# Kernel optimization log

Measured on AMD Instinct MI355X. Metric: run time of the kernel, lower is better.

## Reference

```python
import jax, jax.numpy as jnp
import numpy as np
from jax import lax

EMBED_DIM = 64
NUM_CODES = 512
NUM_HID = 128
NUM_RES_HID = 32
NUM_RES_LAYERS = 2
COMMIT_COST = 0.25
EPS = 1e-5


def conv1d(x, w, b=None, stride=1, pad=0):
    # x: [B,C,L], w: [O,I,K]
    y = lax.conv_general_dilated(x, w, (stride,), [(pad, pad)],
                                 dimension_numbers=('NCH', 'OIH', 'NCH'))
    if b is not None:
        y = y + b[None, :, None]
    return y


def conv_transpose1d(x, w, b, stride=2, pad=1):
    # torch ConvTranspose1d weight: [C_in, C_out, K]; express as fractionally-strided conv
    k = w.shape[-1]
    w2 = jnp.flip(w, axis=-1).transpose(1, 0, 2)  # [C_out, C_in, K]
    y = lax.conv_general_dilated(x, w2, (1,), [(k - 1 - pad, k - 1 - pad)],
                                 lhs_dilation=(stride,),
                                 dimension_numbers=('NCH', 'OIH', 'NCH'))
    return y + b[None, :, None]


def residual_stack(x, res_w1, res_w2):
    # res_w1: [L, R, H, 3], res_w2: [L, H, R, 1]
    for i in range(res_w1.shape[0]):
        h = conv1d(jax.nn.relu(x), res_w1[i], None, 1, 1)
        h = conv1d(jax.nn.relu(h), res_w2[i], None, 1, 0)
        x = x + h
    return jax.nn.relu(x)


def setup_inputs() -> dict:
    key = jax.random.key(0)
    ks = iter(jax.random.split(key, 32))
    B, T = 64, 8192
    H, R, D, K = NUM_HID, NUM_RES_HID, EMBED_DIM, NUM_CODES

    def w(k_, shape, fan_in):
        bound = 1.0 / np.sqrt(fan_in)
        return jax.random.uniform(k_, shape, jnp.float32, -bound, bound)

    inp = {
        'x': jax.random.normal(next(ks), (B, 1, T), jnp.float32),
        # encoder
        'enc_w1': w(next(ks), (H // 2, 1, 4), 1 * 4),
        'enc_b1': w(next(ks), (H // 2,), 1 * 4),
        'enc_w2': w(next(ks), (H, H // 2, 4), (H // 2) * 4),
        'enc_b2': w(next(ks), (H,), (H // 2) * 4),
        'enc_w3': w(next(ks), (H, H, 3), H * 3),
        'enc_b3': w(next(ks), (H,), H * 3),
        'enc_res_w1': w(next(ks), (NUM_RES_LAYERS, R, H, 3), H * 3),
        'enc_res_w2': w(next(ks), (NUM_RES_LAYERS, H, R, 1), R * 1),
        'enc_pre_w': w(next(ks), (D, H, 1), H),
        'enc_pre_b': w(next(ks), (D,), H),
        # codebook
        'codebook': jax.random.uniform(next(ks), (K, D), jnp.float32, -1.0 / K, 1.0 / K),
        # decoder
        'dec_w1': w(next(ks), (H, D, 3), D * 3),
        'dec_b1': w(next(ks), (H,), D * 3),
        'dec_res_w1': w(next(ks), (NUM_RES_LAYERS, R, H, 3), H * 3),
        'dec_res_w2': w(next(ks), (NUM_RES_LAYERS, H, R, 1), R * 1),
        'dec_t1_w': w(next(ks), (H, H // 2, 4), H * 4),   # ConvTranspose1d weight [Cin,Cout,K]
        'dec_t1_b': w(next(ks), (H // 2,), H * 4),
        'dec_t2_w': w(next(ks), (H // 2, 1, 4), (H // 2) * 4),
        'dec_t2_b': w(next(ks), (1,), (H // 2) * 4),
    }
    return inp


def vq_forward(z, codebook):
    # z: [B, D, L]
    B = z.shape[0]
    inputs = z.transpose(0, 2, 1)                       # [B, L, D]
    flat = inputs.reshape(-1, inputs.shape[-1])          # [N, D]
    # squared euclidean distances (argmin equals cdist p=2 argmin)
    d2 = (jnp.sum(flat * flat, axis=1, keepdims=True)
          - 2.0 * flat @ codebook.T
          + jnp.sum(codebook * codebook, axis=1))        # [N, K]
    idx = jnp.argmin(d2, axis=1)                         # [N]
    quant = codebook[idx].reshape(inputs.shape)          # gather == onehot @ codebook

    e_loss = jnp.mean((lax.stop_gradient(quant) - inputs) ** 2)
    q_loss = jnp.mean((quant - lax.stop_gradient(inputs)) ** 2)
    loss = q_loss + COMMIT_COST * e_loss

    quant_st = inputs + lax.stop_gradient(quant - inputs)  # straight-through

    n_tok = flat.shape[0]
    avg_probs = jnp.zeros((codebook.shape[0],), jnp.float32).at[idx].add(1.0) / n_tok
    perplexity = jnp.exp(-jnp.sum(avg_probs * jnp.log(avg_probs + 1e-10)))

    return quant_st.transpose(0, 2, 1), loss, idx.reshape(B, -1), perplexity


def reference(x, enc_w1, enc_b1, enc_w2, enc_b2, enc_w3, enc_b3,
              enc_res_w1, enc_res_w2, enc_pre_w, enc_pre_b, codebook,
              dec_w1, dec_b1, dec_res_w1, dec_res_w2,
              dec_t1_w, dec_t1_b, dec_t2_w, dec_t2_b):
    # RevIN normalize (stats detached)
    means = lax.stop_gradient(jnp.mean(x, axis=2, keepdims=True))
    stds = lax.stop_gradient(jnp.sqrt(jnp.var(x, axis=2, keepdims=True) + EPS))
    xn = (x - means) / stds

    # Encoder
    h = jax.nn.relu(conv1d(xn, enc_w1, enc_b1, 2, 1))
    h = jax.nn.relu(conv1d(h, enc_w2, enc_b2, 2, 1))
    h = conv1d(h, enc_w3, enc_b3, 1, 1)
    h = residual_stack(h, enc_res_w1, enc_res_w2)
    z = conv1d(h, enc_pre_w, enc_pre_b, 1, 0)            # [B, D, T/4]

    # VQ (eval mode: no noise, no EMA)
    quant, vq_loss, indices, perplexity = vq_forward(z, codebook)

    # Decoder
    d = conv1d(quant, dec_w1, dec_b1, 1, 1)
    d = residual_stack(d, dec_res_w1, dec_res_w2)
    d = jax.nn.relu(conv_transpose1d(d, dec_t1_w, dec_t1_b, 2, 1))
    x_recon = conv_transpose1d(d, dec_t2_w, dec_t2_b, 2, 1)

    # RevIN denormalize
    x_recon = x_recon * stds + means
    return x_recon, vq_loss, indices, perplexity
```

## Files before the change

### kernel.cpp

```cpp
#include <hip/hip_runtime.h>
#include <cmath>

#define NBATCH 64
#define NQB    16
#define TLEN   8192
#define LA     4096
#define LB     2048
#define HID    128
#define HHALF  64
#define RESCH  32
#define EMB    64
#define NCODE  512
#define NTOK   (NBATCH * LB)

#define DW_MEAN 0
#define DW_RSTD 64
#define DW_W1   128
#define DW_B1   384
#define DW_W2   448
#define DW_B2   33216
#define DW_W3   33344
#define DW_B3   82496
#define DW_RW1  82624
#define DW_RW2  107200
#define DW_PW   115392
#define DW_PB   123584

#define WS_FMEAN 327680
#define WS_FSTD  327744
#define WS_CNORM 327808
#define WS_CNT   328320
#define WS_SSE   328832

#define OFF_QUANT 2097152ull
#define OFF_D2Q   35651584ull
#define OFF_D3Q   69206016ull
#define OFF_S64Q  102760448ull
#define OFF_Z64Q  111149056ull
#define OFF_A32   69206016ull
#define OFF_S32   2097152ull
#define OFF_B32   2097152ull


__global__ __launch_bounds__(1024) void zero_kernel(float* p, int n) {
    int i = blockIdx.x * 1024 + threadIdx.x;
    if (i < n) p[i] = 0.f;
}

__global__ __launch_bounds__(256) void cvt_kernel(const float* __restrict__ src,
                                                  double* __restrict__ dst, int n) {
    int i = blockIdx.x * 256 + threadIdx.x;
    if (i < n) dst[i] = (double)src[i];
}

__global__ __launch_bounds__(256) void cnorm_kernel(const float* __restrict__ cb,
                                                    float* __restrict__ cnorm) {
    int k = blockIdx.x * 256 + threadIdx.x;
    if (k < NCODE) {
        float p0=0,p1=0,p2=0,p3=0,p4=0,p5=0,p6=0,p7=0;
        const float* cp = cb + k * EMB;
        #pragma unroll
        for (int d = 0; d < EMB; d += 8) {
            p0 = __fadd_rn(p0, __fmul_rn(cp[d],   cp[d]));
            p1 = __fadd_rn(p1, __fmul_rn(cp[d+1], cp[d+1]));
            p2 = __fadd_rn(p2, __fmul_rn(cp[d+2], cp[d+2]));
            p3 = __fadd_rn(p3, __fmul_rn(cp[d+3], cp[d+3]));
            p4 = __fadd_rn(p4, __fmul_rn(cp[d+4], cp[d+4]));
            p5 = __fadd_rn(p5, __fmul_rn(cp[d+5], cp[d+5]));
            p6 = __fadd_rn(p6, __fmul_rn(cp[d+6], cp[d+6]));
            p7 = __fadd_rn(p7, __fmul_rn(cp[d+7], cp[d+7]));
        }
        float s01 = __fadd_rn(p0, p1), s23 = __fadd_rn(p2, p3);
        float s45 = __fadd_rn(p4, p5), s67 = __fadd_rn(p6, p7);
        cnorm[k] = __fadd_rn(__fadd_rn(s01, s23), __fadd_rn(s45, s67));
    }
}

__global__ __launch_bounds__(256) void stats_kernel(const float* __restrict__ x,
                                                    double* dws, float* ws) {
    __shared__ float sx[TLEN];
    __shared__ double red[256];
    const int b = blockIdx.x, t = threadIdx.x;
    const float* xb = x + (size_t)b * TLEN;
    double s = 0.0;
    for (int i = t; i < TLEN; i += 256) { float v = xb[i]; sx[i] = v; s += (double)v; }
    red[t] = s; __syncthreads();
    for (int st = 128; st > 0; st >>= 1) { if (t < st) red[t] += red[t + st]; __syncthreads(); }
    double mean = red[0] / (double)TLEN;
    __syncthreads();
    double s2 = 0.0;
    for (int i = t; i < TLEN; i += 256) { double d = (double)sx[i] - mean; s2 = fma(d, d, s2); }
    red[t] = s2; __syncthreads();
    for (int st = 128; st > 0; st >>= 1) { if (t < st) red[t] += red[t + st]; __syncthreads(); }
    if (t == 0) {
        double stdv = sqrt(red[0] / (double)TLEN + 1e-5);
        dws[DW_MEAN + b] = mean;
        dws[DW_RSTD + b] = 1.0 / stdv;
        ws[WS_FMEAN + b] = (float)mean;
        ws[WS_FSTD + b]  = (float)stdv;
    }
}

__global__ __launch_bounds__(256) void fused12_kern(
        const float* __restrict__ x, const double* __restrict__ dws,
        double* __restrict__ out, int b0) {
    __shared__ double xt[262];
    __shared__ double s1e[64][65];
    __shared__ double s1o[64][65];
    __shared__ double lw1[256];
    __shared__ double lb1[64];
    const int bq = blockIdx.y;
    const int bg = b0 + bq;
    const int l0 = blockIdx.x * 64;
    const int tid = threadIdx.x;
    const double mean = dws[DW_MEAN + bg], rstd = dws[DW_RSTD + bg];
    const double* w2 = dws + DW_W2;
    const double* b2 = dws + DW_B2;

    if (tid < 256) lw1[tid] = dws[DW_W1 + tid];
    if (tid < 64)  lb1[tid] = dws[DW_B1 + tid];
    const int x_base = 4 * l0 - 3;
    const float* xb = x + (size_t)bg * TLEN;
    for (int i = tid; i < 262; i += 256) {
        int g = x_base + i;
        xt[i] = (g >= 0 && g < TLEN) ? ((double)xb[g] - mean) * rstd : 0.0;
    }
    __syncthreads();
    for (int i = tid; i < 64 * 130; i += 256) {
        int o = i / 130, pp = i - o * 130;
        int m = 2 * l0 - 1 + pp;
        double val = 0.0;
        if (m >= 0 && m < LA) {
            double a = lb1[o];
            #pragma unroll
            for (int k = 0; k < 4; k++) a = fma(lw1[o * 4 + k], xt[2 * pp + k], a);
            val = a > 0.0 ? a : 0.0;
        }
        if ((pp & 1) == 0) s1o[o][pp >> 1] = val;
        else               s1e[o][(pp - 1) >> 1] = val;
    }
    __syncthreads();
    const int lane = tid & 63;
    const int wave = tid >> 6;
    const int o0 = __builtin_amdgcn_readfirstlane(wave * 32);
    double acc[32];
    #pragma unroll
    for (int j = 0; j < 32; j++) acc[j] = b2[o0 + j];
    for (int c = 0; c < 64; c++) {
        double v0 = s1o[c][lane];
        double v1 = s1e[c][lane];
        double v2 = s1o[c][lane + 1];
        double v3 = s1e[c][lane + 1];
        #pragma unroll
        for (int j = 0; j < 32; j++) {
            const double* wp = w2 + ((size_t)(o0 + j) * 64 + c) * 4;
            double a = acc[j];
            a = fma(wp[0], v0, a);
            a = fma(wp[1], v1, a);
            a = fma(wp[2], v2, a);
            a = fma(wp[3], v3, a);
            acc[j] = a;
        }
    }
    #pragma unroll
    for (int j = 0; j < 32; j++) {
        double a = acc[j] > 0.0 ? acc[j] : 0.0;
        out[((size_t)bq * HID + o0 + j) * LB + l0 + lane] = a;
    }
}

template<int CIN, int COUT, int K, bool RELU_IN, bool ADD_RES, bool HAS_BIAS>
__global__ __launch_bounds__(256) void conv64_kern(
        const double* __restrict__ in, const double* __restrict__ w,
        const double* __restrict__ bias, const double* res, double* out) {
    constexpr int W = 64 + K - 1;
    __shared__ double st[CIN * W];
    const int b = blockIdx.y;
    const int l0 = blockIdx.x * 64;
    const int tid = threadIdx.x;
    const double* inb = in + (size_t)b * CIN * LB;
    for (int i = tid; i < CIN * W; i += 256) {
        int c = i / W, p = i - c * W;
        int g = l0 + p - (K / 2);
        double v = 0.0;
        if (g >= 0 && g < LB) {
            v = inb[(size_t)c * LB + g];
            if (RELU_IN) v = v > 0.0 ? v : 0.0;
        }
        st[i] = v;
    }
    __syncthreads();
    const int lane = tid & 63;
    const int wave = tid >> 6;
    constexpr int OPW = COUT / 4;
    const int o0 = __builtin_amdgcn_readfirstlane(wave * OPW);
    const int l = l0 + lane;
    double acc[OPW];
    #pragma unroll
    for (int j = 0; j < OPW; j++) acc[j] = HAS_BIAS ? bias[o0 + j] : 0.0;
    for (int c = 0; c < CIN; c++) {
        double v[K];
        #pragma unroll
        for (int k = 0; k < K; k++) v[k] = st[c * W + lane + k];
        #pragma unroll
        for (int j = 0; j < OPW; j++) {
            const double* wp = w + ((size_t)(o0 + j) * CIN + c) * K;
            #pragma unroll
            for (int k = 0; k < K; k++) acc[j] = fma(wp[k], v[k], acc[j]);
        }
    }
    #pragma unroll
    for (int j = 0; j < OPW; j++) {
        double a = acc[j];
        if (ADD_RES) a += res[((size_t)b * COUT + o0 + j) * LB + l];
        out[((size_t)b * COUT + o0 + j) * LB + l] = a;
    }
}

__global__ __launch_bounds__(256) void vq_kernel(
        const double* __restrict__ z64, const float* __restrict__ cbf,
        const float* __restrict__ cnorm,
        float* __restrict__ quant, float* __restrict__ idx_out,
        float* __restrict__ cnt, float* __restrict__ sse_acc, int b0) {
    __shared__ float s_m[4][64];
    __shared__ int   s_c[4][64];
    const int tid = threadIdx.x;
    const int tl = tid & 63;
    const int q = tid >> 6;
    const int nl = blockIdx.x * 64 + tl;
    const int bq = nl >> 11, l = nl & 2047;
    const int bg = b0 + bq;
    const double* zp = z64 + (size_t)bq * EMB * LB + l;
    float zv[EMB];
    #pragma unroll
    for (int d = 0; d < EMB; d++) zv[d] = (float)zp[(size_t)d * LB];

    float p0=0,p1=0,p2=0,p3=0,p4=0,p5=0,p6=0,p7=0;
    #pragma unroll
    for (int d = 0; d < EMB; d += 8) {
        p0 = __fadd_rn(p0, __fmul_rn(zv[d],   zv[d]));
        p1 = __fadd_rn(p1, __fmul_rn(zv[d+1], zv[d+1]));
        p2 = __fadd_rn(p2, __fmul_rn(zv[d+2], zv[d+2]));
        p3 = __fadd_rn(p3, __fmul_rn(zv[d+3], zv[d+3]));
        p4 = __fadd_rn(p4, __fmul_rn(zv[d+4], zv[d+4]));
        p5 = __fadd_rn(p5, __fmul_rn(zv[d+5], zv[d+5]));
        p6 = __fadd_rn(p6, __fmul_rn(zv[d+6], zv[d+6]));
        p7 = __fadd_rn(p7, __fmul_rn(zv[d+7], zv[d+7]));
    }
    const float A = __fadd_rn(__fadd_rn(__fadd_rn(p0,p1), __fadd_rn(p2,p3)),
                              __fadd_rn(__fadd_rn(p4,p5), __fadd_rn(p6,p7)));

    float m1 = 1e30f; int c1 = 0;
    const int c0 = __builtin_amdgcn_readfirstlane(q * 128);
    for (int ci = 0; ci < 128; ci++) {
        const int c = c0 + ci;
        const float* wp = cbf + c * EMB;
        float d0=0,d1=0,d2=0,d3=0,d4=0,d5=0,d6=0,d7=0;
        #pragma unroll
        for (int d = 0; d < EMB; d += 8) {
            d0 = fmaf(wp[d],   zv[d],   d0);
            d1 = fmaf(wp[d+1], zv[d+1], d1);
            d2 = fmaf(wp[d+2], zv[d+2], d2);
            d3 = fmaf(wp[d+3], zv[d+3], d3);
            d4 = fmaf(wp[d+4], zv[d+4], d4);
            d5 = fmaf(wp[d+5], zv[d+5], d5);
            d6 = fmaf(wp[d+6], zv[d+6], d6);
            d7 = fmaf(wp[d+7], zv[d+7], d7);
        }
        float dot = __fadd_rn(__fadd_rn(__fadd_rn(d0,d1), __fadd_rn(d2,d3)),
                              __fadd_rn(__fadd_rn(d4,d5), __fadd_rn(d6,d7)));
        float m = __fadd_rn(__fsub_rn(A, __fmul_rn(2.0f, dot)), cnorm[c]);
        if (m < m1) { m1 = m; c1 = c; }
    }
    s_m[q][tl] = m1; s_c[q][tl] = c1;
    __syncthreads();
    if (q == 0) {
        float bm = s_m[0][tl]; int bc = s_c[0][tl];
        #pragma unroll
        for (int qq = 1; qq < 4; qq++) {
            float mm = s_m[qq][tl];
            if (mm < bm) { bm = mm; bc = s_c[qq][tl]; }
        }
        idx_out[(size_t)bg * LB + l] = (float)bc;
        atomicAdd(&cnt[bc], 1.0f);
        float* qp = quant + (size_t)bg * EMB * LB + l;
        const float* cp = cbf + bc * EMB;
        float sse = 0.f;
        #pragma unroll
        for (int d = 0; d < EMB; d++) {
            float qv = cp[d];
            qp[(size_t)d * LB] = qv;
            float df = qv - zv[d];
            sse = fmaf(df, df, sse);
        }
        for (int off = 32; off > 0; off >>= 1) sse += __shfl_down(sse, off);
        if (tl == 0) atomicAdd(sse_acc, sse);
    }
}

template<int CIN, int COUT, int K, bool RELU_IN, bool RELU_OUT, bool ADD_RES, bool HAS_BIAS>
__global__ __launch_bounds__(256) void conv32_kern(
        const float* __restrict__ in, const float* __restrict__ w,
        const float* __restrict__ bias, const float* res, float* out) {
    constexpr int W = 64 + K - 1;
    __shared__ float st[CIN * W];
    const int b = blockIdx.y;
    const int l0 = blockIdx.x * 64;
    const int tid = threadIdx.x;
    const float* inb = in + (size_t)b * CIN * LB;
    for (int i = tid; i < CIN * W; i += 256) {
        int c = i / W, p = i - c * W;
        int g = l0 + p - (K / 2);
        float v = 0.f;
        if (g >= 0 && g < LB) {
            v = inb[(size_t)c * LB + g];
            if (RELU_IN) v = fmaxf(v, 0.f);
        }
        st[i] = v;
    }
    __syncthreads();
    const int lane = tid & 63;
    const int wave = tid >> 6;
    constexpr int OPW = COUT / 4;
    constexpr int NO = OPW < 16 ? OPW : 16;
    const int l = l0 + lane;
    for (int oc = 0; oc < OPW; oc += NO) {
        const int o0 = __builtin_amdgcn_readfirstlane(wave * OPW + oc);
        float acc[NO];
        #pragma unroll
        for (int j = 0; j < NO; j++) acc[j] = HAS_BIAS ? bias[o0 + j] : 0.f;
        for (int c = 0; c < CIN; c++) {
            float v[K];
            #pragma unroll
            for (int k = 0; k < K; k++) v[k] = st[c * W + lane + k];
            #pragma unroll
            for (int j = 0; j < NO; j++) {
                #pragma unroll
                for (int k = 0; k < K; k++)
                    acc[j] = fmaf(w[((o0 + j) * CIN + c) * K + k], v[k], acc[j]);
            }
        }
        #pragma unroll
        for (int j = 0; j < NO; j++) {
            float a = acc[j];
            if (ADD_RES) a += res[((size_t)b * COUT + o0 + j) * LB + l];
            if (RELU_OUT) a = fmaxf(a, 0.f);
            out[((size_t)b * COUT + o0 + j) * LB + l] = a;
        }
    }
}

__global__ __launch_bounds__(256) void convt1_kern(const float* __restrict__ in,
        const float* __restrict__ w, const float* __restrict__ bias, float* out) {
    __shared__ float s_in[HID * 66];
    const int b = blockIdx.y;
    const int t0 = blockIdx.x * 128;
    const int m0 = t0 / 2 - 1;
    const int tid = threadIdx.x;
    const float* inb = in + (size_t)b * HID * LB;
    for (int i = tid; i < HID * 66; i += 256) {
        int c = i / 66, p = i - c * 66;
        int m = m0 + p;
        s_in[i] = (m >= 0 && m < LB) ? fmaxf(inb[(size_t)c * LB + m], 0.f) : 0.f;
    }
    __syncthreads();
    const int lane = tid & 63;
    const int wave = tid >> 6;
    const int o0 = __builtin_amdgcn_readfirstlane(wave * 16);
    float accE[16], accO[16];
    #pragma unroll
    for (int j = 0; j < 16; j++) { float bv = bias[o0 + j]; accE[j] = bv; accO[j] = bv; }
    for (int c = 0; c < HID; c++) {
        float v0 = s_in[c * 66 + lane];
        float v1 = s_in[c * 66 + lane + 1];
        float v2 = s_in[c * 66 + lane + 2];
        #pragma unroll
        for (int j = 0; j < 16; j++) {
            const float* wc = w + ((size_t)c * HHALF + o0 + j) * 4;
            accE[j] = fmaf(wc[1], v1, fmaf(wc[3], v0, accE[j]));
            accO[j] = fmaf(wc[0], v2, fmaf(wc[2], v1, accO[j]));
        }
    }
    #pragma unroll
    for (int j = 0; j < 16; j++) {
        float2 pr;
        pr.x = fmaxf(accE[j], 0.f);
        pr.y = fmaxf(accO[j], 0.f);
        *(float2*)&out[((size_t)b * HHALF + o0 + j) * LA + t0 + 2 * lane] = pr;
    }
}

__global__ __launch_bounds__(256) void convt2_kern(const float* __restrict__ in,
        const float* __restrict__ w, const float* __restrict__ bias,
        const float* __restrict__ mstats, float* out) {
    __shared__ float s_in[16 * 258];
    const int b = blockIdx.y;
    const int t0 = blockIdx.x * 512;
    const int m0 = t0 / 2 - 1;
    const int tid = threadIdx.x;
    const float* inb = in + (size_t)b * HHALF * LA;
    float accE = 0.f, accO = 0.f;
    for (int cg = 0; cg < 4; cg++) {
        __syncthreads();
        for (int i = tid; i < 16 * 258; i += 256) {
            int c = i / 258, p = i - c * 258;
            int m = m0 + p;
            s_in[i] = (m >= 0 && m < LA) ? inb[(size_t)(cg * 16 + c) * LA + m] : 0.f;
        }
        __syncthreads();
        for (int c = 0; c < 16; c++) {
            float v0 = s_in[c * 258 + tid];
            float v1 = s_in[c * 258 + tid + 1];
            float v2 = s_in[c * 258 + tid + 2];
            const float* wc = w + (size_t)(cg * 16 + c) * 4;
            accE = fmaf(wc[1], v1, fmaf(wc[3], v0, accE));
            accO = fmaf(wc[0], v2, fmaf(wc[2], v1, accO));
        }
    }
    const float mean = mstats[WS_FMEAN + b], stdv = mstats[WS_FSTD + b];
    const float b0 = bias[0];
    float2 pr;
    pr.x = (accE + b0) * stdv + mean;
    pr.y = (accO + b0) * stdv + mean;
    *(float2*)&out[(size_t)b * TLEN + t0 + 2 * tid] = pr;
}

__global__ __launch_bounds__(512) void finalize_kernel(const float* cnt, const float* sse,
                                                       float* d_out) {
    __shared__ float red[512];
    const int t = threadIdx.x;
    float n = cnt[t];
    float p = n / (float)NTOK;
    red[t] = -p * logf(p + 1e-10f);
    __syncthreads();
    for (int s = 256; s > 0; s >>= 1) { if (t < s) red[t] += red[t + s]; __syncthreads(); }
    if (t == 0) {
        d_out[(size_t)NBATCH * TLEN] = sse[0] * 1.25f / (float)((size_t)NTOK * EMB);
        d_out[(size_t)NBATCH * TLEN + 1 + NTOK] = expf(red[0]);
    }
}

extern "C" void kernel_launch(void* const* d_in, const int* in_sizes, int n_in,
                              void* d_out, int out_size, void* d_ws, size_t ws_size,
                              hipStream_t stream) {
    (void)in_sizes; (void)n_in; (void)out_size; (void)ws_size;

    const float* x         = (const float*)d_in[0];
    const float* enc_w1    = (const float*)d_in[1];
    const float* enc_b1    = (const float*)d_in[2];
    const float* enc_w2    = (const float*)d_in[3];
    const float* enc_b2    = (const float*)d_in[4];
    const float* enc_w3    = (const float*)d_in[5];
    const float* enc_b3    = (const float*)d_in[6];
    const float* enc_rw1   = (const float*)d_in[7];
    const float* enc_rw2   = (const float*)d_in[8];
    const float* enc_pre_w = (const float*)d_in[9];
    const float* enc_pre_b = (const float*)d_in[10];
    const float* codebook  = (const float*)d_in[11];
    const float* dec_w1    = (const float*)d_in[12];
    const float* dec_b1    = (const float*)d_in[13];
    const float* dec_rw1   = (const float*)d_in[14];
    const float* dec_rw2   = (const float*)d_in[15];
    const float* dec_t1_w  = (const float*)d_in[16];
    const float* dec_t1_b  = (const float*)d_in[17];
    const float* dec_t2_w  = (const float*)d_in[18];
    const float* dec_t2_b  = (const float*)d_in[19];

    float*  ws  = (float*)d_ws;
    double* dws = (double*)d_ws;
    char*   wsb = (char*)d_ws;
    float*  out = (float*)d_out;

    float*  QUANT = (float*)(wsb + OFF_QUANT);
    double* D2Q   = (double*)(wsb + OFF_D2Q);
    double* D3Q   = (double*)(wsb + OFF_D3Q);
    double* S64Q  = (double*)(wsb + OFF_S64Q);
    double* Z64Q  = (double*)(wsb + OFF_Z64Q);
    float*  A32   = (float*)(wsb + OFF_A32);
    float*  S32   = (float*)(wsb + OFF_S32);
    float*  B32   = (float*)(wsb + OFF_B32);
    float*  idx_out = out + (size_t)NBATCH * TLEN + 1;

    cvt_kernel<<<1, 256, 0, stream>>>(enc_w1, dws + DW_W1, 256);
    cvt_kernel<<<1, 256, 0, stream>>>(enc_b1, dws + DW_B1, 64);
    cvt_kernel<<<128, 256, 0, stream>>>(enc_w2, dws + DW_W2, 32768);
    cvt_kernel<<<1, 256, 0, stream>>>(enc_b2, dws + DW_B2, 128);
    cvt_kernel<<<192, 256, 0, stream>>>(enc_w3, dws + DW_W3, 49152);
    cvt_kernel<<<1, 256, 0, stream>>>(enc_b3, dws + DW_B3, 128);
    cvt_kernel<<<96, 256, 0, stream>>>(enc_rw1, dws + DW_RW1, 24576);
    cvt_kernel<<<32, 256, 0, stream>>>(enc_rw2, dws + DW_RW2, 8192);
    cvt_kernel<<<32, 256, 0, stream>>>(enc_pre_w, dws + DW_PW, 8192);
    cvt_kernel<<<1, 256, 0, stream>>>(enc_pre_b, dws + DW_PB, 64);

    zero_kernel<<<1, 1024, 0, stream>>>(ws + WS_CNT, 513);
    cnorm_kernel<<<2, 256, 0, stream>>>(codebook, ws + WS_CNORM);
    stats_kernel<<<NBATCH, 256, 0, stream>>>(x, dws, ws);

    for (int qq = 0; qq < 4; qq++) {
        const int b0 = qq * NQB;
        fused12_kern<<<dim3(LB / 64, NQB), 256, 0, stream>>>(x, dws, D2Q, b0);
        conv64_kern<128, 128, 3, false, false, true>
            <<<dim3(LB / 64, NQB), 256, 0, stream>>>(D2Q, dws + DW_W3, dws + DW_B3, nullptr, D3Q);
        for (int i = 0; i < 2; i++) {
            conv64_kern<128, 32, 3, true, false, false>
                <<<dim3(LB / 64, NQB), 256, 0, stream>>>(D3Q, dws + DW_RW1 + (size_t)i * 12288,
                                                         nullptr, nullptr, S64Q);
            conv64_kern<32, 128, 1, true, true, false>
                <<<dim3(LB / 64, NQB), 256, 0, stream>>>(S64Q, dws + DW_RW2 + (size_t)i * 4096,
                                                         nullptr, D3Q, D3Q);
        }
        conv64_kern<128, 64, 1, true, false, true>
            <<<dim3(LB / 64, NQB), 256, 0, stream>>>(D3Q, dws + DW_PW, dws + DW_PB, nullptr, Z64Q);
        vq_kernel<<<(NQB * LB) / 64, 256, 0, stream>>>(Z64Q, codebook, ws + WS_CNORM,
                                                       QUANT, idx_out, ws + WS_CNT, ws + WS_SSE, b0);
    }

    conv32_kern<64, 128, 3, false, false, false, true>
        <<<dim3(LB / 64, NBATCH), 256, 0, stream>>>(QUANT, dec_w1, dec_b1, nullptr, A32);
    for (int i = 0; i < 2; i++) {
        conv32_kern<128, 32, 3, true, false, false, false>
            <<<dim3(LB / 64, NBATCH), 256, 0, stream>>>(A32, dec_rw1 + (size_t)i * RESCH * HID * 3,
                                                        nullptr, nullptr, S32);
        conv32_kern<32, 128, 1, true, false, true, false>
            <<<dim3(LB / 64, NBATCH), 256, 0, stream>>>(S32, dec_rw2 + (size_t)i * HID * RESCH,
                                                        nullptr, A32, A32);
    }
    convt1_kern<<<dim3(LA / 128, NBATCH), 256, 0, stream>>>(A32, dec_t1_w, dec_t1_b, B32);
    convt2_kern<<<dim3(TLEN / 512, NBATCH), 256, 0, stream>>>(B32, dec_t2_w, dec_t2_b, ws, out);

    finalize_kernel<<<1, 512, 0, stream>>>(ws + WS_CNT, ws + WS_SSE, out);
}
```

Before: 4.260 ms.

## Run encoder in fp32 instead of fp64 and process full batch at once

Replaces the double-precision encoder path (fused first convs, conv64 kernels, weight conversion kernels) with fp32 kernels reusing the existing conv32 template, and drops the 4-way batch chunking so each stage launches over all 64 batches. This removes the slow fp64 FMA throughput, halves activation memory traffic, and eliminates the cvt launches and chunk loop. It risks changing VQ code assignments where fp32 rounding flips the nearest codebook entry compared with the reference.

After: 3.439 ms. 19.3% less time.

```diff
diff --git a/kernel.cpp b/kernel.cpp
--- a/kernel.cpp
+++ b/kernel.cpp
@@ -2,7 +2,6 @@
 #include <cmath>
 
 #define NBATCH 64
-#define NQB    16
 #define TLEN   8192
 #define LA     4096
 #define LB     2048
@@ -13,44 +12,20 @@
 #define NCODE  512
 #define NTOK   (NBATCH * LB)
 
-#define DW_MEAN 0
-#define DW_RSTD 64
-#define DW_W1   128
-#define DW_B1   384
-#define DW_W2   448
-#define DW_B2   33216
-#define DW_W3   33344
-#define DW_B3   82496
-#define DW_RW1  82624
-#define DW_RW2  107200
-#define DW_PW   115392
-#define DW_PB   123584
-
-#define WS_FMEAN 327680
-#define WS_FSTD  327744
-#define WS_CNORM 327808
-#define WS_CNT   328320
-#define WS_SSE   328832
-
-#define OFF_QUANT 2097152ull
-#define OFF_D2Q   35651584ull
-#define OFF_D3Q   69206016ull
-#define OFF_S64Q  102760448ull
-#define OFF_Z64Q  111149056ull
-#define OFF_A32   69206016ull
-#define OFF_S32   2097152ull
-#define OFF_B32   2097152ull
+#define WS_MEAN  0
+#define WS_RSTD  64
+#define WS_STD   128
+#define WS_CNORM 192
+#define WS_CNT   704
+#define WS_SSE   1216
+#define WS_A     4096
+#define WS_B     (WS_A + 16777216)
+#define WS_S     (WS_B + 16777216)
 
 
 __global__ __launch_bounds__(1024) void zero_kernel(float* p, int n) {
     int i = blockIdx.x * 1024 + threadIdx.x;
     if (i < n) p[i] = 0.f;
-}
-
-__global__ __launch_bounds__(256) void cvt_kernel(const float* __restrict__ src,
-                                                  double* __restrict__ dst, int n) {
-    int i = blockIdx.x * 256 + threadIdx.x;
-    if (i < n) dst[i] = (double)src[i];
 }
 
 __global__ __launch_bounds__(256) void cnorm_kernel(const float* __restrict__ cb,
@@ -76,8 +51,7 @@
     }
 }
 
-__global__ __launch_bounds__(256) void stats_kernel(const float* __restrict__ x,
-                                                    double* dws, float* ws) {
+__global__ __launch_bounds__(256) void stats_kernel(const float* __restrict__ x, float* ws) {
     __shared__ float sx[TLEN];
     __shared__ double red[256];
     const int b = blockIdx.x, t = threadIdx.x;
@@ -94,47 +68,45 @@
     for (int st = 128; st > 0; st >>= 1) { if (t < st) red[t] += red[t + st]; __syncthreads(); }
     if (t == 0) {
         double stdv = sqrt(red[0] / (double)TLEN + 1e-5);
-        dws[DW_MEAN + b] = mean;
-        dws[DW_RSTD + b] = 1.0 / stdv;
-        ws[WS_FMEAN + b] = (float)mean;
-        ws[WS_FSTD + b]  = (float)stdv;
+        ws[WS_MEAN + b] = (float)mean;
+        ws[WS_RSTD + b] = (float)(1.0 / stdv);
+        ws[WS_STD + b]  = (float)stdv;
     }
 }
 
 __global__ __launch_bounds__(256) void fused12_kern(
-        const float* __restrict__ x, const double* __restrict__ dws,
-        double* __restrict__ out, int b0) {
-    __shared__ double xt[262];
-    __shared__ double s1e[64][65];
-    __shared__ double s1o[64][65];
-    __shared__ double lw1[256];
-    __shared__ double lb1[64];
-    const int bq = blockIdx.y;
-    const int bg = b0 + bq;
+        const float* __restrict__ x, const float* __restrict__ w1g,
+        const float* __restrict__ b1g, const float* __restrict__ w2,
+        const float* __restrict__ b2, const float* __restrict__ ws,
+        float* __restrict__ out) {
+    __shared__ float xt[262];
+    __shared__ float s1e[64][65];
+    __shared__ float s1o[64][65];
+    __shared__ float lw1[256];
+    __shared__ float lb1[64];
+    const int b = blockIdx.y;
     const int l0 = blockIdx.x * 64;
     const int tid = threadIdx.x;
-    const double mean = dws[DW_MEAN + bg], rstd = dws[DW_RSTD + bg];
-    const double* w2 = dws + DW_W2;
-    const double* b2 = dws + DW_B2;
-
-    if (tid < 256) lw1[tid] = dws[DW_W1 + tid];
-    if (tid < 64)  lb1[tid] = dws[DW_B1 + tid];
+    const float mean = ws[WS_MEAN + b], stdv = ws[WS_STD + b];
+
+    if (tid < 256) lw1[tid] = w1g[tid];
+    if (tid < 64)  lb1[tid] = b1g[tid];
     const int x_base = 4 * l0 - 3;
-    const float* xb = x + (size_t)bg * TLEN;
+    const float* xb = x + (size_t)b * TLEN;
     for (int i = tid; i < 262; i += 256) {
         int g = x_base + i;
-        xt[i] = (g >= 0 && g < TLEN) ? ((double)xb[g] - mean) * rstd : 0.0;
+        xt[i] = (g >= 0 && g < TLEN) ? (xb[g] - mean) / stdv : 0.f;
     }
     __syncthreads();
     for (int i = tid; i < 64 * 130; i += 256) {
         int o = i / 130, pp = i - o * 130;
         int m = 2 * l0 - 1 + pp;
-        double val = 0.0;
+        float val = 0.f;
         if (m >= 0 && m < LA) {
-            double a = lb1[o];
+            float a = lb1[o];
             #pragma unroll
-            for (int k = 0; k < 4; k++) a = fma(lw1[o * 4 + k], xt[2 * pp + k], a);
-            val = a > 0.0 ? a : 0.0;
+            for (int k = 0; k < 4; k++) a = fmaf(lw1[o * 4 + k], xt[2 * pp + k], a);
+            val = fmaxf(a, 0.f);
         }
         if ((pp & 1) == 0) s1o[o][pp >> 1] = val;
         else               s1e[o][(pp - 1) >> 1] = val;
@@ -143,159 +115,28 @@
     const int lane = tid & 63;
     const int wave = tid >> 6;
     const int o0 = __builtin_amdgcn_readfirstlane(wave * 32);
-    double acc[32];
+    float acc[32];
     #pragma unroll
     for (int j = 0; j < 32; j++) acc[j] = b2[o0 + j];
     for (int c = 0; c < 64; c++) {
-        double v0 = s1o[c][lane];
-        double v1 = s1e[c][lane];
-        double v2 = s1o[c][lane + 1];
-        double v3 = s1e[c][lane + 1];
+        float v0 = s1o[c][lane];
+        float v1 = s1e[c][lane];
+        float v2 = s1o[c][lane + 1];
+        float v3 = s1e[c][lane + 1];
         #pragma unroll
         for (int j = 0; j < 32; j++) {
-            const double* wp = w2 + ((size_t)(o0 + j) * 64 + c) * 4;
-            double a = acc[j];
-            a = fma(wp[0], v0, a);
-            a = fma(wp[1], v1, a);
-            a = fma(wp[2], v2, a);
-            a = fma(wp[3], v3, a);
+            const float* wp = w2 + ((size_t)(o0 + j) * 64 + c) * 4;
+            float a = acc[j];
+            a = fmaf(wp[0], v0, a);
+            a = fmaf(wp[1], v1, a);
+            a = fmaf(wp[2], v2, a);
+            a = fmaf(wp[3], v3, a);
             acc[j] = a;
         }
     }
     #pragma unroll
-    for (int j = 0; j < 32; j++) {
-        double a = acc[j] > 0.0 ? acc[j] : 0.0;
-        out[((size_t)bq * HID + o0 + j) * LB + l0 + lane] = a;
-    }
-}
-
-template<int CIN, int COUT, int K, bool RELU_IN, bool ADD_RES, bool HAS_BIAS>
-__global__ __launch_bounds__(256) void conv64_kern(
-        const double* __restrict__ in, const double* __restrict__ w,
-        const double* __restrict__ bias, const double* res, double* out) {
-    constexpr int W = 64 + K - 1;
-    __shared__ double st[CIN * W];
-    const int b = blockIdx.y;
-    const int l0 = blockIdx.x * 64;
-    const int tid = threadIdx.x;
-    const double* inb = in + (size_t)b * CIN * LB;
-    for (int i = tid; i < CIN * W; i += 256) {
-        int c = i / W, p = i - c * W;
-        int g = l0 + p - (K / 2);
-        double v = 0.0;
-        if (g >= 0 && g < LB) {
-            v = inb[(size_t)c * LB + g];
-            if (RELU_IN) v = v > 0.0 ? v : 0.0;
-        }
-        st[i] = v;
-    }
-    __syncthreads();
-    const int lane = tid & 63;
-    const int wave = tid >> 6;
-    constexpr int OPW = COUT / 4;
-    const int o0 = __builtin_amdgcn_readfirstlane(wave * OPW);
-    const int l = l0 + lane;
-    double acc[OPW];
-    #pragma unroll
-    for (int j = 0; j < OPW; j++) acc[j] = HAS_BIAS ? bias[o0 + j] : 0.0;
-    for (int c = 0; c < CIN; c++) {
-        double v[K];
-        #pragma unroll
-        for (int k = 0; k < K; k++) v[k] = st[c * W + lane + k];
-        #pragma unroll
-        for (int j = 0; j < OPW; j++) {
-            const double* wp = w + ((size_t)(o0 + j) * CIN + c) * K;
-            #pragma unroll
-            for (int k = 0; k < K; k++) acc[j] = fma(wp[k], v[k], acc[j]);
-        }
-    }
-    #pragma unroll
-    for (int j = 0; j < OPW; j++) {
-        double a = acc[j];
-        if (ADD_RES) a += res[((size_t)b * COUT + o0 + j) * LB + l];
-        out[((size_t)b * COUT + o0 + j) * LB + l] = a;
-    }
-}
-
-__global__ __launch_bounds__(256) void vq_kernel(
-        const double* __restrict__ z64, const float* __restrict__ cbf,
-        const float* __restrict__ cnorm,
-        float* __restrict__ quant, float* __restrict__ idx_out,
-        float* __restrict__ cnt, float* __restrict__ sse_acc, int b0) {
-    __shared__ float s_m[4][64];
-    __shared__ int   s_c[4][64];
-    const int tid = threadIdx.x;
-    const int tl = tid & 63;
-    const int q = tid >> 6;
-    const int nl = blockIdx.x * 64 + tl;
-    const int bq = nl >> 11, l = nl & 2047;
-    const int bg = b0 + bq;
-    const double* zp = z64 + (size_t)bq * EMB * LB + l;
-    float zv[EMB];
-    #pragma unroll
-    for (int d = 0; d < EMB; d++) zv[d] = (float)zp[(size_t)d * LB];
-
-    float p0=0,p1=0,p2=0,p3=0,p4=0,p5=0,p6=0,p7=0;
-    #pragma unroll
-    for (int d = 0; d < EMB; d += 8) {
-        p0 = __fadd_rn(p0, __fmul_rn(zv[d],   zv[d]));
-        p1 = __fadd_rn(p1, __fmul_rn(zv[d+1], zv[d+1]));
-        p2 = __fadd_rn(p2, __fmul_rn(zv[d+2], zv[d+2]));
-        p3 = __fadd_rn(p3, __fmul_rn(zv[d+3], zv[d+3]));
-        p4 = __fadd_rn(p4, __fmul_rn(zv[d+4], zv[d+4]));
-        p5 = __fadd_rn(p5, __fmul_rn(zv[d+5], zv[d+5]));
-        p6 = __fadd_rn(p6, __fmul_rn(zv[d+6], zv[d+6]));
-        p7 = __fadd_rn(p7, __fmul_rn(zv[d+7], zv[d+7]));
-    }
-    const float A = __fadd_rn(__fadd_rn(__fadd_rn(p0,p1), __fadd_rn(p2,p3)),
-                              __fadd_rn(__fadd_rn(p4,p5), __fadd_rn(p6,p7)));
-
-    float m1 = 1e30f; int c1 = 0;
-    const int c0 = __builtin_amdgcn_readfirstlane(q * 128);
-    for (int ci = 0; ci < 128; ci++) {
-        const int c = c0 + ci;
-        const float* wp = cbf + c * EMB;
-        float d0=0,d1=0,d2=0,d3=0,d4=0,d5=0,d6=0,d7=0;
-        #pragma unroll
-        for (int d = 0; d < EMB; d += 8) {
-            d0 = fmaf(wp[d],   zv[d],   d0);
-            d1 = fmaf(wp[d+1], zv[d+1], d1);
-            d2 = fmaf(wp[d+2], zv[d+2], d2);
-            d3 = fmaf(wp[d+3], zv[d+3], d3);
-            d4 = fmaf(wp[d+4], zv[d+4], d4);
-            d5 = fmaf(wp[d+5], zv[d+5], d5);
-            d6 = fmaf(wp[d+6], zv[d+6], d6);
-            d7 = fmaf(wp[d+7], zv[d+7], d7);
-        }
-        float dot = __fadd_rn(__fadd_rn(__fadd_rn(d0,d1), __fadd_rn(d2,d3)),
-                              __fadd_rn(__fadd_rn(d4,d5), __fadd_rn(d6,d7)));
-        float m = __fadd_rn(__fsub_rn(A, __fmul_rn(2.0f, dot)), cnorm[c]);
-        if (m < m1) { m1 = m; c1 = c; }
-    }
-    s_m[q][tl] = m1; s_c[q][tl] = c1;
-    __syncthreads();
-    if (q == 0) {
-        float bm = s_m[0][tl]; int bc = s_c[0][tl];
-        #pragma unroll
-        for (int qq = 1; qq < 4; qq++) {
-            float mm = s_m[qq][tl];
-            if (mm < bm) { bm = mm; bc = s_c[qq][tl]; }
-        }
-        idx_out[(size_t)bg * LB + l] = (float)bc;
-        atomicAdd(&cnt[bc], 1.0f);
-        float* qp = quant + (size_t)bg * EMB * LB + l;
-        const float* cp = cbf + bc * EMB;
-        float sse = 0.f;
-        #pragma unroll
-        for (int d = 0; d < EMB; d++) {
-            float qv = cp[d];
-            qp[(size_t)d * LB] = qv;
-            float df = qv - zv[d];
-            sse = fmaf(df, df, sse);
-        }
-        for (int off = 32; off > 0; off >>= 1) sse += __shfl_down(sse, off);
-        if (tl == 0) atomicAdd(sse_acc, sse);
-    }
+    for (int j = 0; j < 32; j++)
+        out[((size_t)b * HID + o0 + j) * LB + l0 + lane] = fmaxf(acc[j], 0.f);
 }
 
 template<int CIN, int COUT, int K, bool RELU_IN, bool RELU_OUT, bool ADD_RES, bool HAS_BIAS>
@@ -350,6 +191,86 @@
     }
 }
 
+__global__ __launch_bounds__(256) void vq_kernel(
+        const float* __restrict__ z, const float* __restrict__ cbf,
+        const float* __restrict__ cnorm,
+        float* __restrict__ quant, float* __restrict__ idx_out,
+        float* __restrict__ cnt, float* __restrict__ sse_acc) {
+    __shared__ float s_m[4][64];
+    __shared__ int   s_c[4][64];
+    const int tid = threadIdx.x;
+    const int tl = tid & 63;
+    const int q = tid >> 6;
+    const int n = blockIdx.x * 64 + tl;
+    const int b = n >> 11, l = n & 2047;
+    const float* zp = z + (size_t)b * EMB * LB + l;
+    float zv[EMB];
+    #pragma unroll
+    for (int d = 0; d < EMB; d++) zv[d] = zp[(size_t)d * LB];
+
+    float p0=0,p1=0,p2=0,p3=0,p4=0,p5=0,p6=0,p7=0;
+    #pragma unroll
+    for (int d = 0; d < EMB; d += 8) {
+        p0 = __fadd_rn(p0, __fmul_rn(zv[d],   zv[d]));
+        p1 = __fadd_rn(p1, __fmul_rn(zv[d+1], zv[d+1]));
+        p2 = __fadd_rn(p2, __fmul_rn(zv[d+2], zv[d+2]));
+        p3 = __fadd_rn(p3, __fmul_rn(zv[d+3], zv[d+3]));
+        p4 = __fadd_rn(p4, __fmul_rn(zv[d+4], zv[d+4]));
+        p5 = __fadd_rn(p5, __fmul_rn(zv[d+5], zv[d+5]));
+        p6 = __fadd_rn(p6, __fmul_rn(zv[d+6], zv[d+6]));
+        p7 = __fadd_rn(p7, __fmul_rn(zv[d+7], zv[d+7]));
+    }
+    const float A = __fadd_rn(__fadd_rn(__fadd_rn(p0,p1), __fadd_rn(p2,p3)),
+                              __fadd_rn(__fadd_rn(p4,p5), __fadd_rn(p6,p7)));
+
+    float m1 = 1e30f; int c1 = 0;
+    const int c0 = __builtin_amdgcn_readfirstlane(q * 128);
+    for (int ci = 0; ci < 128; ci++) {
+        const int c = c0 + ci;
+        const float* wp = cbf + c * EMB;
+        float d0=0,d1=0,d2=0,d3=0,d4=0,d5=0,d6=0,d7=0;
+        #pragma unroll
+        for (int d = 0; d < EMB; d += 8) {
+            d0 = fmaf(wp[d],   zv[d],   d0);
+            d1 = fmaf(wp[d+1], zv[d+1], d1);
+            d2 = fmaf(wp[d+2], zv[d+2], d2);
+            d3 = fmaf(wp[d+3], zv[d+3], d3);
+            d4 = fmaf(wp[d+4], zv[d+4], d4);
+            d5 = fmaf(wp[d+5], zv[d+5], d5);
+            d6 = fmaf(wp[d+6], zv[d+6], d6);
+            d7 = fmaf(wp[d+7], zv[d+7], d7);
+        }
+        float dot = __fadd_rn(__fadd_rn(__fadd_rn(d0,d1), __fadd_rn(d2,d3)),
+                              __fadd_rn(__fadd_rn(d4,d5), __fadd_rn(d6,d7)));
+        float m = __fadd_rn(__fsub_rn(A, __fmul_rn(2.0f, dot)), cnorm[c]);
+        if (m < m1) { m1 = m; c1 = c; }
+    }
+    s_m[q][tl] = m1; s_c[q][tl] = c1;
+    __syncthreads();
+    if (q == 0) {
+        float bm = s_m[0][tl]; int bc = s_c[0][tl];
+        #pragma unroll
+        for (int qq = 1; qq < 4; qq++) {
+            float mm = s_m[qq][tl];
+            if (mm < bm) { bm = mm; bc = s_c[qq][tl]; }
+        }
+        idx_out[n] = (float)bc;
+        atomicAdd(&cnt[bc], 1.0f);
+        float* qp = quant + (size_t)b * EMB * LB + l;
+        const float* cp = cbf + bc * EMB;
+        float sse = 0.f;
+        #pragma unroll
+        for (int d = 0; d < EMB; d++) {
+            float qv = cp[d];
+            qp[(size_t)d * LB] = qv;
+            float df = qv - zv[d];
+            sse = fmaf(df, df, sse);
+        }
+        for (int off = 32; off > 0; off >>= 1) sse += __shfl_down(sse, off);
+        if (tl == 0) atomicAdd(sse_acc, sse);
+    }
+}
+
 __global__ __launch_bounds__(256) void convt1_kern(const float* __restrict__ in,
         const float* __restrict__ w, const float* __restrict__ bias, float* out) {
     __shared__ float s_in[HID * 66];
@@ -417,7 +338,7 @@
             accO = fmaf(wc[0], v2, fmaf(wc[2], v1, accO));
         }
     }
-    const float mean = mstats[WS_FMEAN + b], stdv = mstats[WS_FSTD + b];
+    const float mean = mstats[WS_MEAN + b], stdv = mstats[WS_STD + b];
     const float b0 = bias[0];
     float2 pr;
     pr.x = (accE + b0) * stdv + mean;
@@ -466,67 +387,49 @@
     const float* dec_t2_w  = (const float*)d_in[18];
     const float* dec_t2_b  = (const float*)d_in[19];
 
-    float*  ws  = (float*)d_ws;
-    double* dws = (double*)d_ws;
-    char*   wsb = (char*)d_ws;
-    float*  out = (float*)d_out;
-
-    float*  QUANT = (float*)(wsb + OFF_QUANT);
-    double* D2Q   = (double*)(wsb + OFF_D2Q);
-    double* D3Q   = (double*)(wsb + OFF_D3Q);
-    double* S64Q  = (double*)(wsb + OFF_S64Q);
-    double* Z64Q  = (double*)(wsb + OFF_Z64Q);
-    float*  A32   = (float*)(wsb + OFF_A32);
-    float*  S32   = (float*)(wsb + OFF_S32);
-    float*  B32   = (float*)(wsb + OFF_B32);
-    float*  idx_out = out + (size_t)NBATCH * TLEN + 1;
-
-    cvt_kernel<<<1, 256, 0, stream>>>(enc_w1, dws + DW_W1, 256);
-    cvt_kernel<<<1, 256, 0, stream>>>(enc_b1, dws + DW_B1, 64);
-    cvt_kernel<<<128, 256, 0, stream>>>(enc_w2, dws + DW_W2, 32768);
-    cvt_kernel<<<1, 256, 0, stream>>>(enc_b2, dws + DW_B2, 128);
-    cvt_kernel<<<192, 256, 0, stream>>>(enc_w3, dws + DW_W3, 49152);
-    cvt_kernel<<<1, 256, 0, stream>>>(enc_b3, dws + DW_B3, 128);
-    cvt_kernel<<<96, 256, 0, stream>>>(enc_rw1, dws + DW_RW1, 24576);
-    cvt_kernel<<<32, 256, 0, stream>>>(enc_rw2, dws + DW_RW2, 8192);
-    cvt_kernel<<<32, 256, 0, stream>>>(enc_pre_w, dws + DW_PW, 8192);
-    cvt_kernel<<<1, 256, 0, stream>>>(enc_pre_b, dws + DW_PB, 64);
+    float* ws  = (float*)d_ws;
+    float* out = (float*)d_out;
+    float* A   = ws + WS_A;
+    float* Bb  = ws + WS_B;
+    float* S   = ws + WS_S;
+    float* z     = Bb;
+    float* quant = Bb + (size_t)NBATCH * EMB * LB;
+    float* idx_out = out + (size_t)NBATCH * TLEN + 1;
 
     zero_kernel<<<1, 1024, 0, stream>>>(ws + WS_CNT, 513);
     cnorm_kernel<<<2, 256, 0, stream>>>(codebook, ws + WS_CNORM);
-    stats_kernel<<<NBATCH, 256, 0, stream>>>(x, dws, ws);
-
-    for (int qq = 0; qq < 4; qq++) {
-        const int b0 = qq * NQB;
-        fused12_kern<<<dim3(LB / 64, NQB), 256, 0, stream>>>(x, dws, D2Q, b0);
-        conv64_kern<128, 128, 3, false, false, true>
-            <<<dim3(LB / 64, NQB), 256, 0, stream>>>(D2Q, dws + DW_W3, dws + DW_B3, nullptr, D3Q);
-        for (int i = 0; i < 2; i++) {
-            conv64_kern<128, 32, 3, true, false, false>
-                <<<dim3(LB / 64, NQB), 256, 0, stream>>>(D3Q, dws + DW_RW1 + (size_t)i * 12288,
-                                                         nullptr, nullptr, S64Q);
-            conv64_kern<32, 128, 1, true, true, false>
-                <<<dim3(LB / 64, NQB), 256, 0, stream>>>(S64Q, dws + DW_RW2 + (size_t)i * 4096,
-                                                         nullptr, D3Q, D3Q);
-        }
-        conv64_kern<128, 64, 1, true, false, true>
-            <<<dim3(LB / 64, NQB), 256, 0, stream>>>(D3Q, dws + DW_PW, dws + DW_PB, nullptr, Z64Q);
-        vq_kernel<<<(NQB * LB) / 64, 256, 0, stream>>>(Z64Q, codebook, ws + WS_CNORM,
-                                                       QUANT, idx_out, ws + WS_CNT, ws + WS_SSE, b0);
-    }
-
-    conv32_kern<64, 128, 3, false, false, false, true>
-        <<<dim3(LB / 64, NBATCH), 256, 0, stream>>>(QUANT, dec_w1, dec_b1, nullptr, A32);
+    stats_kernel<<<NBATCH, 256, 0, stream>>>(x, ws);
+
+    fused12_kern<<<dim3(LB / 64, NBATCH), 256, 0, stream>>>(x, enc_w1, enc_b1,
+                                                            enc_w2, enc_b2, ws, Bb);
+    conv32_kern<128, 128, 3, false, false, false, true>
+        <<<dim3(LB / 64, NBATCH), 256, 0, stream>>>(Bb, enc_w3, enc_b3, nullptr, A);
     for (int i = 0; i < 2; i++) {
         conv32_kern<128, 32, 3, true, false, false, false>
-            <<<dim3(LB / 64, NBATCH), 256, 0, stream>>>(A32, dec_rw1 + (size_t)i * RESCH * HID * 3,
-                                                        nullptr, nullptr, S32);
+            <<<dim3(LB / 64, NBATCH), 256, 0, stream>>>(A, enc_rw1 + (size_t)i * RESCH * HID * 3,
+                                                        nullptr, nullptr, S);
         conv32_kern<32, 128, 1, true, false, true, false>
-            <<<dim3(LB / 64, NBATCH), 256, 0, stream>>>(S32, dec_rw2 + (size_t)i * HID * RESCH,
-                                                        nullptr, A32, A32);
-    }
-    convt1_kern<<<dim3(LA / 128, NBATCH), 256, 0, stream>>>(A32, dec_t1_w, dec_t1_b, B32);
-    convt2_kern<<<dim3(TLEN / 512, NBATCH), 256, 0, stream>>>(B32, dec_t2_w, dec_t2_b, ws, out);
+            <<<dim3(LB / 64, NBATCH), 256, 0, stream>>>(S, enc_rw2 + (size_t)i * HID * RESCH,
+                                                        nullptr, A, A);
+    }
+    conv32_kern<128, 64, 1, true, false, false, true>
+        <<<dim3(LB / 64, NBATCH), 256, 0, stream>>>(A, enc_pre_w, enc_pre_b, nullptr, z);
+
+    vq_kernel<<<NTOK / 64, 256, 0, stream>>>(z, codebook, ws + WS_CNORM,
+                                             quant, idx_out, ws + WS_CNT, ws + WS_SSE);
+
+    conv32_kern<64, 128, 3, false, false, false, true>
+        <<<dim3(LB / 64, NBATCH), 256, 0, stream>>>(quant, dec_w1, dec_b1, nullptr, A);
+    for (int i = 0; i < 2; i++) {
+        conv32_kern<128, 32, 3, true, false, false, false>
+            <<<dim3(LB / 64, NBATCH), 256, 0, stream>>>(A, dec_rw1 + (size_t)i * RESCH * HID * 3,
+                                                        nullptr, nullptr, S);
+        conv32_kern<32, 128, 1, true, false, true, false>
+            <<<dim3(LB / 64, NBATCH), 256, 0, stream>>>(S, dec_rw2 + (size_t)i * HID * RESCH,
+                                                        nullptr, A, A);
+    }
+    convt1_kern<<<dim3(LA / 128, NBATCH), 256, 0, stream>>>(A, dec_t1_w, dec_t1_b, Bb);
+    convt2_kern<<<dim3(TLEN / 512, NBATCH), 256, 0, stream>>>(Bb, dec_t2_w, dec_t2_b, ws, out);
 
     finalize_kernel<<<1, 512, 0, stream>>>(ws + WS_CNT, ws + WS_SSE, out);
 }
```
